# Optimization experiments

Hardware: AMD Instinct MI355X
Metric: run time of the kernel (lower is better)

Reference implementation:

```python
import jax, jax.numpy as jnp
import numpy as np

N_NODES = 50000
N_EDGES = 800000
D_IN = 512
D_OUT = 128


def setup_inputs() -> dict:
    key = jax.random.key(0)
    k1, k2, k3, k4, k5 = jax.random.split(key, 5)
    x = jax.random.normal(k1, (N_NODES, D_IN), dtype=jnp.float32)
    edge_src = jax.random.randint(k2, (N_EDGES,), 0, N_NODES, dtype=jnp.int32)
    edge_dst = jnp.sort(jax.random.randint(k3, (N_EDGES,), 0, N_NODES, dtype=jnp.int32))
    edge_val = jax.random.uniform(k4, (N_EDGES,), dtype=jnp.float32)
    stdv = 1.0 / np.sqrt(D_OUT)
    weight = jax.random.uniform(k5, (D_IN, D_OUT), dtype=jnp.float32,
                                minval=-stdv, maxval=stdv)
    return {"x": x, "edge_src": edge_src, "edge_dst": edge_dst,
            "edge_val": edge_val, "weight": weight}


def reference(x, edge_src, edge_dst, edge_val, weight):
    # support = X @ W : dense GEMM [N, D_in] x [D_in, D_out]
    support = x @ weight
    # output = A @ support : SpMM via gather + weighted segment-sum over dst
    gathered = support[edge_src] * edge_val[:, None]  # [E, D_out]
    output = jax.ops.segment_sum(gathered, edge_dst, num_segments=x.shape[0])
    return output
```

## Files before the change

### kernel.cpp

```cpp
#include <hip/hip_runtime.h>
#include <hip/hip_bf16.h>

#define M_NODES 50000
#define K_DIM   512
#define N_DIM   128

typedef short s16x8 __attribute__((ext_vector_type(8)));
typedef float f32x4 __attribute__((ext_vector_type(4)));

static __device__ __forceinline__ ushort f2bf(float f) {
  uint u = __float_as_uint(f);
  u += 0x7fff + ((u >> 16) & 1);
  return (ushort)(u >> 16);
}

static __device__ __forceinline__ uint cvtpk(float lo, float hi) {
  uint r;
  asm("v_cvt_pk_bf16_f32 %0, %1, %2" : "=v"(r) : "v"(lo), "v"(hi));
  return r;
}

static __device__ __forceinline__ void g2l16(const void* g, void* l) {
  __builtin_amdgcn_global_load_lds((const __attribute__((address_space(1))) void*)g,
                                   (__attribute__((address_space(3))) void*)l, 16, 0, 0);
}

__global__ __launch_bounds__(256) void prep_zero(const float* __restrict__ W,
                                                 ushort* __restrict__ Wt,
                                                 float4* __restrict__ o4, int n4) {
  const int t = blockIdx.x * 256 + threadIdx.x;
  const int stride = gridDim.x * 256;
  for (int i = t; i < n4; i += stride) o4[i] = make_float4(0.f, 0.f, 0.f, 0.f);
  if (t < 16384) {
    int k  = t >> 5;
    int c0 = (t & 31) * 4;
    float4 v = *reinterpret_cast<const float4*>(&W[(size_t)k * N_DIM + c0]);
    Wt[(size_t)(c0 + 0) * K_DIM + k] = f2bf(v.x);
    Wt[(size_t)(c0 + 1) * K_DIM + k] = f2bf(v.y);
    Wt[(size_t)(c0 + 2) * K_DIM + k] = f2bf(v.z);
    Wt[(size_t)(c0 + 3) * K_DIM + k] = f2bf(v.w);
  }
}

#define GBK 32
#define NKS (K_DIM / GBK)

__global__ __launch_bounds__(256, 4) void gemm_mfma(const float* __restrict__ X,
                                                    const ushort* __restrict__ Wt,
                                                    ushort* __restrict__ Sb) {
  __shared__ float  Albs[2][64 * 32];
  __shared__ ushort Blbs[2][128 * 32];

  const int tid = threadIdx.x;
  const int w   = tid >> 6;
  const int l   = tid & 63;
  const int l15 = l & 15, lg = l >> 4;
  const int wr  = w >> 1, wc = w & 1;
  const int row0 = blockIdx.x * 64;

  const float* aSrc[2];
#pragma unroll
  for (int i = 0; i < 2; ++i) {
    int q = i * 256 + w * 64 + l;
    int r = q >> 3;
    int c = (q & 7) ^ (r & 7);
    int rg = row0 + r; if (rg >= M_NODES) rg = M_NODES - 1;
    aSrc[i] = X + (size_t)rg * K_DIM + c * 4;
  }
  const ushort* bSrc[2];
#pragma unroll
  for (int i = 0; i < 2; ++i) {
    int q = i * 256 + w * 64 + l;
    int col = q >> 2, j = q & 3;
    bSrc[i] = Wt + (size_t)col * K_DIM + j * 8;
  }

  f32x4 acc[2][4];
#pragma unroll
  for (int am = 0; am < 2; ++am)
#pragma unroll
    for (int bn = 0; bn < 4; ++bn) acc[am][bn] = (f32x4){0.f, 0.f, 0.f, 0.f};

#define STAGE(buf, kk) { \
  _Pragma("unroll") for (int i = 0; i < 2; ++i) \
    g2l16(aSrc[i] + (kk), (char*)&Albs[buf][0] + (size_t)(i * 256 + w * 64) * 16); \
  _Pragma("unroll") for (int i = 0; i < 2; ++i) \
    g2l16(bSrc[i] + (kk), (char*)&Blbs[buf][0] + (size_t)(i * 256 + w * 64) * 16); }

#define COMPUTE(buf) { \
  s16x8 af[2], bfr[4]; \
  _Pragma("unroll") for (int am = 0; am < 2; ++am) { \
    const int r = wr * 32 + am * 16 + l15; \
    const int s = r & 7; \
    float4 f0 = *reinterpret_cast<const float4*>(&Albs[buf][(r * 8 + ((lg * 2) ^ s)) * 4]); \
    float4 f1 = *reinterpret_cast<const float4*>(&Albs[buf][(r * 8 + ((lg * 2 + 1) ^ s)) * 4]); \
    union { s16x8 v; uint u[4]; } a; \
    a.u[0] = cvtpk(f0.x, f0.y); a.u[1] = cvtpk(f0.z, f0.w); \
    a.u[2] = cvtpk(f1.x, f1.y); a.u[3] = cvtpk(f1.z, f1.w); \
    af[am] = a.v; } \
  _Pragma("unroll") for (int bn = 0; bn < 4; ++bn) { \
    const int c = wc * 64 + bn * 16 + l15; \
    bfr[bn] = *reinterpret_cast<const s16x8*>(&Blbs[buf][c * 32 + lg * 8]); } \
  _Pragma("unroll") for (int am = 0; am < 2; ++am) \
    _Pragma("unroll") for (int bn = 0; bn < 4; ++bn) \
      acc[am][bn] = __builtin_amdgcn_mfma_f32_16x16x32_bf16(af[am], bfr[bn], acc[am][bn], 0, 0, 0); }

  STAGE(0, 0)
  __syncthreads();
#pragma unroll
  for (int t = 0; t < NKS; ++t) {
    if (t + 1 < NKS) STAGE((t + 1) & 1, (t + 1) * GBK)
    COMPUTE(t & 1)
    __syncthreads();
  }
#undef STAGE
#undef COMPUTE

#pragma unroll
  for (int am = 0; am < 2; ++am) {
#pragma unroll
    for (int rr = 0; rr < 4; ++rr) {
      const int row = row0 + wr * 32 + am * 16 + lg * 4 + rr;
      if (row < M_NODES) {
        ushort* sp = Sb + (size_t)row * N_DIM + wc * 64 + l15;
#pragma unroll
        for (int bn = 0; bn < 4; ++bn)
          sp[bn * 16] = f2bf(acc[am][bn][rr]);
      }
    }
  }
}

#define EPB 256
#define CPW 128
#define SB 32

__global__ __launch_bounds__(128, 4) void spmm_edges(const ushort* __restrict__ Sb,
                                                     const int* __restrict__ esrc,
                                                     const int* __restrict__ edst,
                                                     const float* __restrict__ eval,
                                                     float* __restrict__ out) {
  __shared__ int   s_src[EPB];
  __shared__ int   s_dst[EPB];
  __shared__ float s_val[EPB];

  const int e0  = blockIdx.x * EPB;
  const int tid = threadIdx.x;

#pragma unroll
  for (int i = 0; i < EPB / 128; ++i) {
    int idx = tid + i * 128;
    s_src[idx] = esrc[e0 + idx];
    s_dst[idx] = edst[e0 + idx];
    s_val[idx] = eval[e0 + idx];
  }
  __syncthreads();

  const int w    = tid >> 6;
  const int l    = tid & 63;
  const int base = w * CPW;
  const uint colb = (uint)l * 4u;

  const int first = s_dst[base];
  int   cur = first;
  float ax = 0.f, ay = 0.f;

  uint bufA[SB], bufB[SB];

#define SLOAD(BUF, B) { \
  _Pragma("unroll") for (int j = 0; j < SB; ++j) \
    BUF[j] = *reinterpret_cast<const uint*>( \
        (const char*)Sb + (size_t)s_src[base + (B) * SB + j] * 256 + colb); }

#define FLUSH() { \
  float* op = out + (size_t)cur * N_DIM + l * 2; \
  if (cur == first) { atomicAdd(op, ax); atomicAdd(op + 1, ay); } \
  else { *reinterpret_cast<float2*>(op) = make_float2(ax, ay); } \
  ax = 0.f; ay = 0.f; }

#define SPROC(BUF, B) { \
  _Pragma("unroll") for (int j = 0; j < SB; ++j) { \
    const int e = base + (B) * SB + j; \
    const int d = s_dst[e]; \
    if (d != cur) { FLUSH() cur = d; } \
    const float vv = s_val[e]; \
    const float lo = __uint_as_float(BUF[j] << 16); \
    const float hi = __uint_as_float(BUF[j] & 0xffff0000u); \
    ax += vv * lo; ay += vv * hi; } }

  SLOAD(bufA, 0)
#pragma unroll
  for (int b = 0; b < CPW / SB; b += 2) {
    if (b + 1 < CPW / SB) SLOAD(bufB, b + 1)
    SPROC(bufA, b)
    if (b + 2 < CPW / SB) SLOAD(bufA, b + 2)
    SPROC(bufB, b + 1)
  }
  {
    float* op = out + (size_t)cur * N_DIM + l * 2;
    atomicAdd(op, ax); atomicAdd(op + 1, ay);
  }
#undef SLOAD
#undef SPROC
#undef FLUSH
}

extern "C" void kernel_launch(void* const* d_in, const int* in_sizes, int n_in,
                              void* d_out, int out_size, void* d_ws, size_t ws_size,
                              hipStream_t stream) {
  const float* x        = (const float*)d_in[0];
  const int*   edge_src = (const int*)d_in[1];
  const int*   edge_dst = (const int*)d_in[2];
  const float* edge_val = (const float*)d_in[3];
  const float* weight   = (const float*)d_in[4];
  float*       out      = (float*)d_out;

  ushort* sb = (ushort*)d_ws;
  ushort* wt = (ushort*)((char*)d_ws + (size_t)M_NODES * N_DIM * 2);

  const int n_edges = in_sizes[1];

  prep_zero<<<dim3(512), dim3(256), 0, stream>>>(weight, wt, (float4*)d_out,
                                                 out_size / 4);

  gemm_mfma<<<dim3((M_NODES + 63) / 64), dim3(256), 0, stream>>>(x, wt, sb);

  spmm_edges<<<dim3(n_edges / EPB), dim3(128), 0, stream>>>(sb, edge_src,
                                                            edge_dst, edge_val, out);
}
```

Before: 214.1 us.

## Stage gathered SpMM rows into LDS via async global_load_lds double buffering

The SpMM kernel no longer gathers source rows into large register arrays with per-lane 4-byte loads. Each wave now issues 16-byte global_load_lds copies of whole bf16 rows into a per-wave double-buffered LDS area, waits with explicit vmcnt counts, and reads its column pair back from LDS. The aim is wider, more coalesced gather transactions, lower register pressure and overlap of the next batch's loads with the current batch's compute. The cost is extra LDS traffic and shallower prefetch (16 edges per batch instead of 32), and correctness rests on hand-written waitcnt values matching the number of loads in flight.

```diff
diff --git a/kernel.cpp b/kernel.cpp
--- a/kernel.cpp
+++ b/kernel.cpp
@@ -133,13 +133,15 @@
 
 #define EPB 256
 #define CPW 128
-#define SB 32
+#define EB  16
+#define NBATCH (CPW / EB)
 
 __global__ __launch_bounds__(128, 4) void spmm_edges(const ushort* __restrict__ Sb,
                                                      const int* __restrict__ esrc,
                                                      const int* __restrict__ edst,
                                                      const float* __restrict__ eval,
                                                      float* __restrict__ out) {
+  __shared__ ushort rows[2][2][EB * 128];
   __shared__ int   s_src[EPB];
   __shared__ int   s_dst[EPB];
   __shared__ float s_val[EPB];
@@ -159,18 +161,16 @@
   const int w    = tid >> 6;
   const int l    = tid & 63;
   const int base = w * CPW;
-  const uint colb = (uint)l * 4u;
 
   const int first = s_dst[base];
   int   cur = first;
   float ax = 0.f, ay = 0.f;
 
-  uint bufA[SB], bufB[SB];
-
-#define SLOAD(BUF, B) { \
-  _Pragma("unroll") for (int j = 0; j < SB; ++j) \
-    BUF[j] = *reinterpret_cast<const uint*>( \
-        (const char*)Sb + (size_t)s_src[base + (B) * SB + j] * 256 + colb); }
+#define SSTAGE(buf, b) { \
+  _Pragma("unroll") for (int i = 0; i < EB / 4; ++i) { \
+    const int er = base + (b) * EB + i * 4 + (l >> 4); \
+    const char* src = (const char*)Sb + (size_t)s_src[er] * 256 + (l & 15) * 16; \
+    g2l16(src, (char*)&rows[w][buf][0] + i * 1024); } }
 
 #define FLUSH() { \
   float* op = out + (size_t)cur * N_DIM + l * 2; \
@@ -178,30 +178,34 @@
   else { *reinterpret_cast<float2*>(op) = make_float2(ax, ay); } \
   ax = 0.f; ay = 0.f; }
 
-#define SPROC(BUF, B) { \
-  _Pragma("unroll") for (int j = 0; j < SB; ++j) { \
-    const int e = base + (B) * SB + j; \
+#define SPROCB(buf, b) { \
+  _Pragma("unroll") for (int j = 0; j < EB; ++j) { \
+    const int e = base + (b) * EB + j; \
     const int d = s_dst[e]; \
     if (d != cur) { FLUSH() cur = d; } \
     const float vv = s_val[e]; \
-    const float lo = __uint_as_float(BUF[j] << 16); \
-    const float hi = __uint_as_float(BUF[j] & 0xffff0000u); \
-    ax += vv * lo; ay += vv * hi; } }
-
-  SLOAD(bufA, 0)
-#pragma unroll
-  for (int b = 0; b < CPW / SB; b += 2) {
-    if (b + 1 < CPW / SB) SLOAD(bufB, b + 1)
-    SPROC(bufA, b)
-    if (b + 2 < CPW / SB) SLOAD(bufA, b + 2)
-    SPROC(bufB, b + 1)
+    const uint pv = *reinterpret_cast<const uint*>(&rows[w][buf][j * 128 + l * 2]); \
+    ax += vv * __uint_as_float(pv << 16); \
+    ay += vv * __uint_as_float(pv & 0xffff0000u); } }
+
+  SSTAGE(0, 0)
+#pragma unroll
+  for (int b = 0; b < NBATCH; ++b) {
+    if (b + 1 < NBATCH) {
+      SSTAGE((b + 1) & 1, b + 1)
+      asm volatile("s_waitcnt vmcnt(4)" ::: "memory");
+    } else {
+      asm volatile("s_waitcnt vmcnt(0)" ::: "memory");
+    }
+    __builtin_amdgcn_sched_barrier(0);
+    SPROCB(b & 1, b)
   }
   {
     float* op = out + (size_t)cur * N_DIM + l * 2;
     atomicAdd(op, ax); atomicAdd(op + 1, ay);
   }
-#undef SLOAD
-#undef SPROC
+#undef SSTAGE
+#undef SPROCB
 #undef FLUSH
 }
 
```

Measured after the change: 213.2 us. Within noise of the previous version (-0.5%).
